# Kernel optimization log

Measured on AMD Instinct MI355X. Metric: run time of the kernel, lower is better.

The kernel has to match this reference:

```python
import jax, jax.numpy as jnp
import numpy as np

B, L, CIN, C = 256, 65, 2053, 512
SCALE = 1.0 / float(np.sqrt(C))


def _attn_layer(x, Wq, bq, Wk, bk, Wv, bv):
    # x: [B, Cin, L]; Conv1d(kernel=1) == channel-mixing matmul
    q = jnp.einsum('oi,bil->bol', Wq, x) + bq[:, None]
    k = jnp.einsum('oi,bil->bol', Wk, x) + bk[:, None]
    v = jax.nn.leaky_relu(jnp.einsum('oi,bil->bol', Wv, x) + bv[:, None], 0.01)
    # att[b,l,m] = <q[:,l], k[:,m]> / sqrt(C); softmax over m
    att = jax.nn.softmax(jnp.einsum('bcl,bcm->blm', q, k) * SCALE, axis=-1)
    # original: sum_m att[b,l,1,m] * v[b,1,c,m] -> [B,L,C] -> permute -> [B,C,L]
    out = jnp.einsum('blm,bcm->bcl', att, v)
    return out + x if out.shape == x.shape else out  # residual only when channels match


def _transform(x, Wq0, bq0, Wk0, bk0, Wv0, bv0, Wq, bq, Wk, bk, Wv, bv):
    x = _attn_layer(x, Wq0, bq0, Wk0, bk0, Wv0, bv0)
    for n in range(3):  # layers 1..3, C->C with residual
        x = _attn_layer(x, Wq[n], bq[n], Wk[n], bk[n], Wv[n], bv[n])
    return x


def setup_inputs():
    key = jax.random.key(0)
    ks = jax.random.split(key, 20)
    s = 0.02
    inp = {
        'dataleft': jax.random.normal(ks[0], (B, L, CIN), jnp.float32),
        'dataright': jax.random.normal(ks[1], (B, L, CIN), jnp.float32),
        # layer-0 QKV conv1d (k=1) weights: [C, CIN]
        'Wq0': jax.random.normal(ks[2], (C, CIN), jnp.float32) * s,
        'bq0': jnp.zeros((C,), jnp.float32),
        'Wk0': jax.random.normal(ks[3], (C, CIN), jnp.float32) * s,
        'bk0': jnp.zeros((C,), jnp.float32),
        'Wv0': jax.random.normal(ks[4], (C, CIN), jnp.float32) * s,
        'bv0': jnp.zeros((C,), jnp.float32),
        # layers 1..3 stacked: [3, C, C]
        'Wq': jax.random.normal(ks[5], (3, C, C), jnp.float32) * s,
        'bq': jnp.zeros((3, C), jnp.float32),
        'Wk': jax.random.normal(ks[6], (3, C, C), jnp.float32) * s,
        'bk': jnp.zeros((3, C), jnp.float32),
        'Wv': jax.random.normal(ks[7], (3, C, C), jnp.float32) * s,
        'bv': jnp.zeros((3, C), jnp.float32),
        # classifier: fc1(1024->256), fc2(256->2)
        'W1': jax.random.normal(ks[8], (256, 2 * C), jnp.float32) * s,
        'b1': jnp.zeros((256,), jnp.float32),
        'W2': jax.random.normal(ks[9], (2, 256), jnp.float32) * s,
        'b2': jnp.zeros((2,), jnp.float32),
    }
    return inp


def reference(dataleft, dataright, Wq0, bq0, Wk0, bk0, Wv0, bv0,
              Wq, bq, Wk, bk, Wv, bv, W1, b1, W2, b2):
    xl = jnp.transpose(dataleft, (0, 2, 1))   # [B, CIN, L]
    xr = jnp.transpose(dataright, (0, 2, 1))
    xl = _transform(xl, Wq0, bq0, Wk0, bk0, Wv0, bv0, Wq, bq, Wk, bk, Wv, bv)
    xr = _transform(xr, Wq0, bq0, Wk0, bk0, Wv0, bv0, Wq, bq, Wk, bk, Wv, bv)
    # AdaptiveAvgPool2d((512,1)) on [B,512,L]: identity over channel dim, mean over L
    xl = jnp.mean(xl, axis=-1)  # [B, C]
    xr = jnp.mean(xr, axis=-1)
    h = jnp.concatenate([xl, xr], axis=1)            # [B, 2C]
    h = jax.nn.relu(h @ W1.T + b1)                   # [B, 256]
    y = h @ W2.T + b2                                # [B, 2]
    return y  # training mode: no final softmax
```

## Files before the change

kernel.cpp:

```cpp
#include <hip/hip_runtime.h>
#include <hip/hip_bf16.h>

#define BF16 __hip_bfloat16

typedef __bf16 bf16x8 __attribute__((ext_vector_type(8)));
typedef float f32x4 __attribute__((ext_vector_type(4)));

__device__ __forceinline__ void async_copy16(const void* g, void* l) {
    __builtin_amdgcn_global_load_lds(
        (const __attribute__((address_space(1))) void*)g,
        (__attribute__((address_space(3))) void*)l,
        16, 0, 0);
}

__global__ __launch_bounds__(256) void convert_pad_k(
    const float* __restrict__ src, BF16* __restrict__ dst,
    long pairs, int Ks, int Kd) {
    long p = (long)blockIdx.x * blockDim.x + threadIdx.x;
    if (p >= pairs) return;
    long e = p * 2;
    long r = e / Kd;
    int k = (int)(e - r * Kd);
    float a = (k < Ks) ? src[r * Ks + k] : 0.f;
    float b = (k + 1 < Ks) ? src[r * Ks + k + 1] : 0.f;
    dst[e] = __float2bfloat16(a);
    dst[e + 1] = __float2bfloat16(b);
}

__global__ __launch_bounds__(256, 3) void gemm_qkv(
    const BF16* __restrict__ Xg, const BF16* __restrict__ Wg,
    const float* __restrict__ bqp, const float* __restrict__ bkp, const float* __restrict__ bvp,
    BF16* __restrict__ Qo, BF16* __restrict__ Ko, BF16* __restrict__ Vo,
    int K, int vtmode) {
    __shared__ __align__(16) BF16 Xs[2][128 * 32];
    __shared__ __align__(16) BF16 Ws[2][128 * 32];
    const int tid = threadIdx.x;
    const int w = tid >> 6;
    const int lane = tid & 63;
    const int quad = lane >> 4;
    const int l15 = lane & 15;
    const long n0 = (long)blockIdx.y * 128;
    const int m0full = blockIdx.x * 128;
    const int sel = blockIdx.x >> 2;
    const int mbase = (blockIdx.x & 3) * 128;
    const int wn = (w & 1) * 64;
    const int wm = (w >> 1) * 64;
    const int srow = lane >> 2;
    const int skoff = (lane & 3) * 8;
    f32x4 acc[4][4] = {};
    for (int k0 = 0; k0 < K; k0 += 64) {
#pragma unroll
        for (int sub = 0; sub < 2; ++sub) {
#pragma unroll
            for (int c = 0; c < 2; ++c) {
                const int rbase = w * 32 + c * 16;
                const int kcol = k0 + sub * 32 + skoff;
                async_copy16(Xg + (n0 + rbase + srow) * K + kcol, &Xs[sub][rbase * 32]);
                async_copy16(Wg + (long)(m0full + rbase + srow) * K + kcol, &Ws[sub][rbase * 32]);
            }
        }
        __syncthreads();
#pragma unroll
        for (int sub = 0; sub < 2; ++sub) {
            bf16x8 af[4], bfr[4];
#pragma unroll
            for (int i = 0; i < 4; ++i)
                af[i] = *(const bf16x8*)&Xs[sub][(wn + i * 16 + l15) * 32 + quad * 8];
#pragma unroll
            for (int j = 0; j < 4; ++j)
                bfr[j] = *(const bf16x8*)&Ws[sub][(wm + j * 16 + l15) * 32 + quad * 8];
#pragma unroll
            for (int i = 0; i < 4; ++i)
#pragma unroll
                for (int j = 0; j < 4; ++j)
                    acc[i][j] = __builtin_amdgcn_mfma_f32_16x16x32_bf16(af[i], bfr[j], acc[i][j], 0, 0, 0);
        }
        __syncthreads();
    }
    const float* bp = (sel == 0) ? bqp : (sel == 1) ? bkp : bvp;
    BF16* out = (sel == 0) ? Qo : (sel == 1) ? Ko : Vo;
#pragma unroll
    for (int j = 0; j < 4; ++j) {
        const int m = mbase + wm + j * 16 + l15;
        const float bz = bp[m];
#pragma unroll
        for (int i = 0; i < 4; ++i) {
#pragma unroll
            for (int r = 0; r < 4; ++r) {
                const long n = n0 + wn + i * 16 + quad * 4 + r;
                float v = acc[i][j][r] + bz;
                if (sel == 2) {
                    v = (v >= 0.f) ? v : 0.01f * v;
                    if (vtmode) {
                        const int ni = (int)n;
                        const int bb = ni / 65;
                        const int l = ni - bb * 65;
                        out[((long)bb * 512 + m) * 96 + l] = __float2bfloat16(v);
                        continue;
                    }
                }
                out[n * 512 + m] = __float2bfloat16(v);
            }
        }
    }
}

__global__ __launch_bounds__(256) void vtrans_k(const ushort* __restrict__ Vb,
                                                ushort* __restrict__ Vt) {
    const int bb = blockIdx.x;
    for (int idx = threadIdx.x; idx < 512 * 33; idx += 256) {
        const int c = idx / 33;
        const int m = (idx - c * 33) * 2;
        ushort a = Vb[((long)bb * 65 + m) * 512 + c];
        ushort b = (m + 1 < 65) ? Vb[((long)bb * 65 + m + 1) * 512 + c] : (ushort)0;
        *(uint*)&Vt[((long)bb * 512 + c) * 96 + m] = (uint)a | ((uint)b << 16);
    }
}

__global__ __launch_bounds__(256) void attn_scores(
    const BF16* __restrict__ Qg, const BF16* __restrict__ Kg, BF16* __restrict__ Pg) {
    constexpr float SC = 0.04419417382415922f;
    __shared__ __align__(16) BF16 Qs[2][80 * 32];
    __shared__ __align__(16) BF16 Ks[2][80 * 32];
    __shared__ float Sf[80 * 84];
    const int bb = blockIdx.x;
    const int tid = threadIdx.x;
    const int w = tid >> 6, lane = tid & 63, quad = lane >> 4, l15 = lane & 15;
    int i16[7], j16[7], nt = 0;
    for (int t = w; t < 25; t += 4) {
        i16[nt] = (t / 5) * 16;
        j16[nt] = (t % 5) * 16;
        ++nt;
    }
    f32x4 acc[7] = {};
    for (int k0 = 0; k0 < 512; k0 += 64) {
        for (int idx = tid; idx < 1280; idx += 256) {
            const int t = (idx >= 640) ? 1 : 0;
            const int e = idx - t * 640;
            const int sub = (e >= 320) ? 1 : 0;
            const int e2 = e - sub * 320;
            const int row = e2 >> 2;
            const int koff = (e2 & 3) * 8;
            uint4 val = make_uint4(0, 0, 0, 0);
            if (row < 65) {
                const BF16* src = (t ? Kg : Qg) + ((long)(bb * 65 + row) * 512 + k0 + sub * 32 + koff);
                val = *(const uint4*)src;
            }
            *(uint4*)&((t ? Ks : Qs)[sub][row * 32 + koff]) = val;
        }
        __syncthreads();
#pragma unroll
        for (int sub = 0; sub < 2; ++sub) {
            for (int u = 0; u < nt; ++u) {
                bf16x8 af = *(const bf16x8*)&Qs[sub][(i16[u] + l15) * 32 + quad * 8];
                bf16x8 bfr = *(const bf16x8*)&Ks[sub][(j16[u] + l15) * 32 + quad * 8];
                acc[u] = __builtin_amdgcn_mfma_f32_16x16x32_bf16(af, bfr, acc[u], 0, 0, 0);
            }
        }
        __syncthreads();
    }
    for (int u = 0; u < nt; ++u)
#pragma unroll
        for (int r = 0; r < 4; ++r)
            Sf[(i16[u] + quad * 4 + r) * 84 + j16[u] + l15] = acc[u][r] * SC;
    __syncthreads();
    for (int rr = tid >> 2; rr < 65; rr += 64) {
        const int sub = tid & 3;
        float mx = -1e30f;
        for (int m = sub; m < 65; m += 4) mx = fmaxf(mx, Sf[rr * 84 + m]);
        mx = fmaxf(mx, __shfl_xor(mx, 1));
        mx = fmaxf(mx, __shfl_xor(mx, 2));
        float s = 0.f;
        for (int m = sub; m < 65; m += 4) {
            float e = __expf(Sf[rr * 84 + m] - mx);
            Sf[rr * 84 + m] = e;
            s += e;
        }
        s += __shfl_xor(s, 1);
        s += __shfl_xor(s, 2);
        const float inv = 1.f / s;
        const long base = ((long)bb * 65 + rr) * 96;
        for (int m = sub; m < 96; m += 4) {
            float v = (m < 65) ? Sf[rr * 84 + m] * inv : 0.f;
            Pg[base + m] = __float2bfloat16(v);
        }
    }
}

__global__ __launch_bounds__(256) void attn_pv(
    const BF16* __restrict__ Pg, const BF16* __restrict__ Vt,
    BF16* __restrict__ Xg, int residual) {
    __shared__ __align__(16) BF16 Ps[80 * 104];
    const int bb = blockIdx.x;
    const int c0 = blockIdx.y * 128;
    const int tid = threadIdx.x;
    const int w = tid >> 6, lane = tid & 63, quad = lane >> 4, l15 = lane & 15;
    for (int idx = tid; idx < 960; idx += 256) {
        const int row = idx / 12;
        const int kk = idx - row * 12;
        uint4 val = make_uint4(0, 0, 0, 0);
        if (row < 65) val = *(const uint4*)(Pg + ((long)bb * 65 + row) * 96 + kk * 8);
        *(uint4*)&Ps[row * 104 + kk * 8] = val;
    }
    __syncthreads();
    bf16x8 af[5][3];
#pragma unroll
    for (int i = 0; i < 5; ++i)
#pragma unroll
        for (int ks = 0; ks < 3; ++ks)
            af[i][ks] = *(const bf16x8*)&Ps[(i * 16 + l15) * 104 + ks * 32 + quad * 8];
#pragma unroll
    for (int jj = 0; jj < 2; ++jj) {
        const int c = c0 + (jj * 4 + w) * 16 + l15;
        const BF16* vp = Vt + ((long)bb * 512 + c) * 96 + quad * 8;
        bf16x8 b0 = *(const bf16x8*)vp;
        bf16x8 b1 = *(const bf16x8*)(vp + 32);
        bf16x8 b2 = *(const bf16x8*)(vp + 64);
        f32x4 po[5] = {};
#pragma unroll
        for (int i = 0; i < 5; ++i) {
            po[i] = __builtin_amdgcn_mfma_f32_16x16x32_bf16(af[i][0], b0, po[i], 0, 0, 0);
            po[i] = __builtin_amdgcn_mfma_f32_16x16x32_bf16(af[i][1], b1, po[i], 0, 0, 0);
            po[i] = __builtin_amdgcn_mfma_f32_16x16x32_bf16(af[i][2], b2, po[i], 0, 0, 0);
        }
#pragma unroll
        for (int i = 0; i < 5; ++i)
#pragma unroll
            for (int r = 0; r < 4; ++r) {
                const int l = i * 16 + quad * 4 + r;
                if (l < 65) {
                    const long idx = ((long)(bb * 65 + l)) * 512 + c;
                    float v = po[i][r];
                    if (residual) v += __bfloat162float(Xg[idx]);
                    Xg[idx] = __float2bfloat16(v);
                }
            }
    }
}

__global__ __launch_bounds__(256) void pool_k(const BF16* __restrict__ Xg,
                                              float* __restrict__ Hp) {
    const int sb = blockIdx.x;
    const int s = sb >> 8, b = sb & 255;
    for (int c = threadIdx.x; c < 512; c += 256) {
        float acc = 0.f;
        for (int l = 0; l < 65; ++l)
            acc += __bfloat162float(Xg[((long)sb * 65 + l) * 512 + c]);
        Hp[(long)b * 1024 + s * 512 + c] = acc * (1.f / 65.f);
    }
}

__global__ __launch_bounds__(256) void fc_k(
    const float* __restrict__ Hp, const float* __restrict__ W1,
    const float* __restrict__ b1, const float* __restrict__ W2,
    const float* __restrict__ b2, float* __restrict__ out) {
    __shared__ float h[1024];
    __shared__ float h1[256];
    const int b = blockIdx.x, tid = threadIdx.x;
    for (int k = tid; k < 1024; k += 256) h[k] = Hp[(long)b * 1024 + k];
    __syncthreads();
    float acc = b1[tid];
    for (int k = 0; k < 1024; ++k) acc += W1[(long)tid * 1024 + k] * h[k];
    h1[tid] = fmaxf(acc, 0.f);
    __syncthreads();
    const int w = tid >> 6, lane = tid & 63;
    if (w < 2) {
        float p = 0.f;
        for (int u = lane; u < 256; u += 64) p += W2[w * 256 + u] * h1[u];
        for (int off = 32; off > 0; off >>= 1) p += __shfl_down(p, off);
        if (lane == 0) out[b * 2 + w] = p + b2[w];
    }
}

extern "C" void kernel_launch(void* const* d_in, const int* in_sizes, int n_in,
                              void* d_out, int out_size, void* d_ws, size_t ws_size,
                              hipStream_t stream) {
    const float* dataL = (const float*)d_in[0];
    const float* dataR = (const float*)d_in[1];
    const float* Wq0 = (const float*)d_in[2];
    const float* bq0 = (const float*)d_in[3];
    const float* Wk0 = (const float*)d_in[4];
    const float* bk0 = (const float*)d_in[5];
    const float* Wv0 = (const float*)d_in[6];
    const float* bv0 = (const float*)d_in[7];
    const float* Wq = (const float*)d_in[8];
    const float* bq = (const float*)d_in[9];
    const float* Wk = (const float*)d_in[10];
    const float* bk = (const float*)d_in[11];
    const float* Wv = (const float*)d_in[12];
    const float* bv = (const float*)d_in[13];
    const float* W1 = (const float*)d_in[14];
    const float* b1 = (const float*)d_in[15];
    const float* W2 = (const float*)d_in[16];
    const float* b2 = (const float*)d_in[17];

    char* ws = (char*)d_ws;
    BF16* Xb = (BF16*)ws;
    BF16* X = Xb;
    BF16* Vt = (BF16*)(ws + 34078720L);
    BF16* Pg = (BF16*)(ws + 84410368L);
    float* Hp = (float*)(ws + 90800128L);
    BF16* Wc = (BF16*)(ws + 140574720L);
    BF16* Qb = (BF16*)(ws + 151781376L);
    BF16* Kb = (BF16*)(ws + 185860096L);
    BF16* Vb = (BF16*)(ws + 219938816L);

    BF16* w0 = Wc;
    BF16* wl = Wc + 3L * 512 * 2112;

    auto cvt = [&](const float* src, BF16* dst, long R, int Ks, int Kd) {
        long pairs = R * Kd / 2;
        int blocks = (int)((pairs + 255) / 256);
        convert_pad_k<<<blocks, 256, 0, stream>>>(src, dst, pairs, Ks, Kd);
    };
    cvt(dataL, Xb, 16640, 2053, 2112);
    cvt(dataR, Xb + 16640L * 2112, 16640, 2053, 2112);
    cvt(Wq0, w0, 512, 2053, 2112);
    cvt(Wk0, w0 + 512L * 2112, 512, 2053, 2112);
    cvt(Wv0, w0 + 2L * 512 * 2112, 512, 2053, 2112);
    for (int n = 0; n < 3; ++n) {
        BF16* base = wl + (long)n * 3 * 262144;
        cvt(Wq + (long)n * 262144, base, 512, 512, 512);
        cvt(Wk + (long)n * 262144, base + 262144, 512, 512, 512);
        cvt(Wv + (long)n * 262144, base + 2 * 262144, 512, 512, 512);
    }

    dim3 ggrid(12, 260);
    dim3 pvgrid(512, 4);
    gemm_qkv<<<ggrid, 256, 0, stream>>>(Xb, w0, bq0, bk0, bv0, Qb, Kb, Vb, 2112, 0);
    vtrans_k<<<512, 256, 0, stream>>>((const ushort*)Vb, (ushort*)Vt);
    attn_scores<<<512, 256, 0, stream>>>(Qb, Kb, Pg);
    attn_pv<<<pvgrid, 256, 0, stream>>>(Pg, Vt, X, 0);
    for (int n = 0; n < 3; ++n) {
        gemm_qkv<<<ggrid, 256, 0, stream>>>(X, wl + (long)n * 3 * 262144,
                                            bq + n * 512, bk + n * 512, bv + n * 512,
                                            Qb, Kb, Vt, 512, 1);
        attn_scores<<<512, 256, 0, stream>>>(Qb, Kb, Pg);
        attn_pv<<<pvgrid, 256, 0, stream>>>(Pg, Vt, X, 1);
    }
    pool_k<<<512, 256, 0, stream>>>(X, Hp);
    fc_k<<<256, 256, 0, stream>>>(Hp, W1, b1, W2, b2, (float*)d_out);
}
```

Before: 1.430 ms.

## Fuse attention scores, softmax and PV into a single-wave per-batch kernel

Replaces the separate attn_scores and attn_pv kernels with one 64-thread kernel per batch element. It computes QK^T in registers straight from global memory, runs the softmax with lane shuffles, and stages unnormalized probabilities in LDS. Normalization is deferred to the PV output stage. This removes the Pg global round trip, one launch per layer and the LDS staging of Q and K, at the cost of far fewer waves in flight and heavier per-wave work.

```diff
diff --git a/kernel.cpp b/kernel.cpp
--- a/kernel.cpp
+++ b/kernel.cpp
@@ -117,90 +117,72 @@
     }
 }
 
-__global__ __launch_bounds__(256) void attn_scores(
-    const BF16* __restrict__ Qg, const BF16* __restrict__ Kg, BF16* __restrict__ Pg) {
+__global__ __launch_bounds__(64) void attn_wave(
+    const BF16* __restrict__ Qg, const BF16* __restrict__ Kg,
+    const BF16* __restrict__ Vt, BF16* __restrict__ Xg, int residual) {
     constexpr float SC = 0.04419417382415922f;
-    __shared__ __align__(16) BF16 Qs[2][80 * 32];
-    __shared__ __align__(16) BF16 Ks[2][80 * 32];
-    __shared__ float Sf[80 * 84];
-    const int bb = blockIdx.x;
-    const int tid = threadIdx.x;
-    const int w = tid >> 6, lane = tid & 63, quad = lane >> 4, l15 = lane & 15;
-    int i16[7], j16[7], nt = 0;
-    for (int t = w; t < 25; t += 4) {
-        i16[nt] = (t / 5) * 16;
-        j16[nt] = (t % 5) * 16;
-        ++nt;
-    }
-    f32x4 acc[7] = {};
-    for (int k0 = 0; k0 < 512; k0 += 64) {
-        for (int idx = tid; idx < 1280; idx += 256) {
-            const int t = (idx >= 640) ? 1 : 0;
-            const int e = idx - t * 640;
-            const int sub = (e >= 320) ? 1 : 0;
-            const int e2 = e - sub * 320;
-            const int row = e2 >> 2;
-            const int koff = (e2 & 3) * 8;
-            uint4 val = make_uint4(0, 0, 0, 0);
-            if (row < 65) {
-                const BF16* src = (t ? Kg : Qg) + ((long)(bb * 65 + row) * 512 + k0 + sub * 32 + koff);
-                val = *(const uint4*)src;
-            }
-            *(uint4*)&((t ? Ks : Qs)[sub][row * 32 + koff]) = val;
-        }
-        __syncthreads();
-#pragma unroll
-        for (int sub = 0; sub < 2; ++sub) {
-            for (int u = 0; u < nt; ++u) {
-                bf16x8 af = *(const bf16x8*)&Qs[sub][(i16[u] + l15) * 32 + quad * 8];
-                bf16x8 bfr = *(const bf16x8*)&Ks[sub][(j16[u] + l15) * 32 + quad * 8];
-                acc[u] = __builtin_amdgcn_mfma_f32_16x16x32_bf16(af, bfr, acc[u], 0, 0, 0);
-            }
-        }
-        __syncthreads();
-    }
-    for (int u = 0; u < nt; ++u)
-#pragma unroll
-        for (int r = 0; r < 4; ++r)
-            Sf[(i16[u] + quad * 4 + r) * 84 + j16[u] + l15] = acc[u][r] * SC;
-    __syncthreads();
-    for (int rr = tid >> 2; rr < 65; rr += 64) {
-        const int sub = tid & 3;
-        float mx = -1e30f;
-        for (int m = sub; m < 65; m += 4) mx = fmaxf(mx, Sf[rr * 84 + m]);
-        mx = fmaxf(mx, __shfl_xor(mx, 1));
-        mx = fmaxf(mx, __shfl_xor(mx, 2));
-        float s = 0.f;
-        for (int m = sub; m < 65; m += 4) {
-            float e = __expf(Sf[rr * 84 + m] - mx);
-            Sf[rr * 84 + m] = e;
-            s += e;
-        }
-        s += __shfl_xor(s, 1);
-        s += __shfl_xor(s, 2);
-        const float inv = 1.f / s;
-        const long base = ((long)bb * 65 + rr) * 96;
-        for (int m = sub; m < 96; m += 4) {
-            float v = (m < 65) ? Sf[rr * 84 + m] * inv : 0.f;
-            Pg[base + m] = __float2bfloat16(v);
-        }
-    }
-}
-
-__global__ __launch_bounds__(256) void attn_pv(
-    const BF16* __restrict__ Pg, const BF16* __restrict__ Vt,
-    BF16* __restrict__ Xg, int residual) {
     __shared__ __align__(16) BF16 Ps[80 * 104];
     const int bb = blockIdx.x;
-    const int c0 = blockIdx.y * 128;
-    const int tid = threadIdx.x;
-    const int w = tid >> 6, lane = tid & 63, quad = lane >> 4, l15 = lane & 15;
-    for (int idx = tid; idx < 960; idx += 256) {
-        const int row = idx / 12;
-        const int kk = idx - row * 12;
-        uint4 val = make_uint4(0, 0, 0, 0);
-        if (row < 65) val = *(const uint4*)(Pg + ((long)bb * 65 + row) * 96 + kk * 8);
-        *(uint4*)&Ps[row * 104 + kk * 8] = val;
+    const int lane = threadIdx.x & 63;
+    const int quad = lane >> 4, l15 = lane & 15;
+    for (int e = lane; e < 1040; e += 64) ((uint4*)Ps)[e] = make_uint4(0, 0, 0, 0);
+    long qrow[5], krow[5];
+#pragma unroll
+    for (int i = 0; i < 5; ++i) {
+        int r = i * 16 + l15;
+        r = (r < 65) ? r : 0;
+        qrow[i] = ((long)bb * 65 + r) * 512;
+        krow[i] = qrow[i];
+    }
+    f32x4 acc[25] = {};
+#pragma unroll 4
+    for (int k0 = 0; k0 < 512; k0 += 32) {
+        bf16x8 qa[5], kb[5];
+#pragma unroll
+        for (int i = 0; i < 5; ++i) qa[i] = *(const bf16x8*)(Qg + qrow[i] + k0 + quad * 8);
+#pragma unroll
+        for (int j = 0; j < 5; ++j) kb[j] = *(const bf16x8*)(Kg + krow[j] + k0 + quad * 8);
+#pragma unroll
+        for (int i = 0; i < 5; ++i)
+#pragma unroll
+            for (int j = 0; j < 5; ++j)
+                acc[i * 5 + j] = __builtin_amdgcn_mfma_f32_16x16x32_bf16(qa[i], kb[j], acc[i * 5 + j], 0, 0, 0);
+    }
+    __syncthreads();
+    float invv[5][4];
+#pragma unroll
+    for (int i = 0; i < 5; ++i) {
+#pragma unroll
+        for (int r = 0; r < 4; ++r) {
+            float s0 = acc[i * 5 + 0][r] * SC;
+            float s1 = acc[i * 5 + 1][r] * SC;
+            float s2 = acc[i * 5 + 2][r] * SC;
+            float s3 = acc[i * 5 + 3][r] * SC;
+            float s4 = acc[i * 5 + 4][r] * SC;
+            float mx = fmaxf(fmaxf(s0, s1), fmaxf(s2, s3));
+            mx = fmaxf(mx, (l15 == 0) ? s4 : -1e30f);
+            mx = fmaxf(mx, __shfl_xor(mx, 1));
+            mx = fmaxf(mx, __shfl_xor(mx, 2));
+            mx = fmaxf(mx, __shfl_xor(mx, 4));
+            mx = fmaxf(mx, __shfl_xor(mx, 8));
+            float e0 = __expf(s0 - mx), e1 = __expf(s1 - mx);
+            float e2 = __expf(s2 - mx), e3 = __expf(s3 - mx);
+            float e4 = (l15 == 0) ? __expf(s4 - mx) : 0.f;
+            float sum = e0 + e1 + e2 + e3 + e4;
+            sum += __shfl_xor(sum, 1);
+            sum += __shfl_xor(sum, 2);
+            sum += __shfl_xor(sum, 4);
+            sum += __shfl_xor(sum, 8);
+            invv[i][r] = 1.f / sum;
+            const int row = i * 16 + quad * 4 + r;
+            if (row < 65) {
+                Ps[row * 104 + 0 * 16 + l15] = __float2bfloat16(e0);
+                Ps[row * 104 + 1 * 16 + l15] = __float2bfloat16(e1);
+                Ps[row * 104 + 2 * 16 + l15] = __float2bfloat16(e2);
+                Ps[row * 104 + 3 * 16 + l15] = __float2bfloat16(e3);
+                if (l15 == 0) Ps[row * 104 + 64] = __float2bfloat16(e4);
+            }
+        }
     }
     __syncthreads();
     bf16x8 af[5][3];
@@ -209,10 +191,11 @@
 #pragma unroll
         for (int ks = 0; ks < 3; ++ks)
             af[i][ks] = *(const bf16x8*)&Ps[(i * 16 + l15) * 104 + ks * 32 + quad * 8];
-#pragma unroll
-    for (int jj = 0; jj < 2; ++jj) {
-        const int c = c0 + (jj * 4 + w) * 16 + l15;
-        const BF16* vp = Vt + ((long)bb * 512 + c) * 96 + quad * 8;
+    const long vbase = (long)bb * 512 * 96;
+#pragma unroll 2
+    for (int jt = 0; jt < 32; ++jt) {
+        const int c = jt * 16 + l15;
+        const BF16* vp = Vt + vbase + (long)c * 96 + quad * 8;
         bf16x8 b0 = *(const bf16x8*)vp;
         bf16x8 b1 = *(const bf16x8*)(vp + 32);
         bf16x8 b2 = *(const bf16x8*)(vp + 64);
@@ -227,10 +210,10 @@
         for (int i = 0; i < 5; ++i)
 #pragma unroll
             for (int r = 0; r < 4; ++r) {
-                const int l = i * 16 + quad * 4 + r;
-                if (l < 65) {
-                    const long idx = ((long)(bb * 65 + l)) * 512 + c;
-                    float v = po[i][r];
+                const int row = i * 16 + quad * 4 + r;
+                if (row < 65) {
+                    const long idx = ((long)bb * 65 + row) * 512 + c;
+                    float v = po[i][r] * invv[i][r];
                     if (residual) v += __bfloat162float(Xg[idx]);
                     Xg[idx] = __float2bfloat16(v);
                 }
@@ -298,7 +281,6 @@
     BF16* Xb = (BF16*)ws;
     BF16* X = Xb;
     BF16* Vt = (BF16*)(ws + 34078720L);
-    BF16* Pg = (BF16*)(ws + 84410368L);
     float* Hp = (float*)(ws + 90800128L);
     BF16* Wc = (BF16*)(ws + 140574720L);
     BF16* Qb = (BF16*)(ws + 151781376L);
@@ -326,17 +308,14 @@
     }
 
     dim3 ggrid(12, 260);
-    dim3 pvgrid(512, 4);
     gemm_qkv<<<ggrid, 256, 0, stream>>>(Xb, w0, bq0, bk0, bv0, Qb, Kb, Vb, 2112, 0);
     vtrans_k<<<512, 256, 0, stream>>>((const ushort*)Vb, (ushort*)Vt);
-    attn_scores<<<512, 256, 0, stream>>>(Qb, Kb, Pg);
-    attn_pv<<<pvgrid, 256, 0, stream>>>(Pg, Vt, X, 0);
+    attn_wave<<<512, 64, 0, stream>>>(Qb, Kb, Vt, X, 0);
     for (int n = 0; n < 3; ++n) {
         gemm_qkv<<<ggrid, 256, 0, stream>>>(X, wl + (long)n * 3 * 262144,
                                             bq + n * 512, bk + n * 512, bv + n * 512,
                                             Qb, Kb, Vt, 512, 1);
-        attn_scores<<<512, 256, 0, stream>>>(Qb, Kb, Pg);
-        attn_pv<<<pvgrid, 256, 0, stream>>>(Pg, Vt, X, 1);
+        attn_wave<<<512, 64, 0, stream>>>(Qb, Kb, Vt, X, 1);
     }
     pool_k<<<512, 256, 0, stream>>>(X, Hp);
     fc_k<<<256, 256, 0, stream>>>(Hp, W1, b1, W2, b2, (float*)d_out);
```

Result: slower. 1.592 ms (+11.4%).
